# Optimization experiments

Hardware: AMD Instinct MI355X
Metric: run time of the kernel (lower is better)

## Reference

```python
import jax, jax.numpy as jnp
import numpy as np

T, B, I, H = 2048, 64, 256, 256

def setup_inputs() -> dict:
    key = jax.random.key(0)
    k_x, k_wih, k_whh = jax.random.split(key, 3)
    x = jax.random.normal(k_x, (T, B, I), dtype=jnp.float32)
    h0 = jnp.zeros((1, B, H), dtype=jnp.float32)
    # nn.RNN weight_ih_l0 init: U(-1/sqrt(H), 1/sqrt(H)); shape [H, I]
    bound = 1.0 / np.sqrt(H)
    W_ih = jax.random.uniform(k_wih, (H, I), minval=-bound, maxval=bound, dtype=jnp.float32)
    # IndRNN recurrent weight: diagonal vector, U(-1, 1); biases are zeroed.
    w_hh = jax.random.uniform(k_whh, (H,), minval=-1.0, maxval=1.0, dtype=jnp.float32)
    return {"x": x, "h0": h0, "W_ih": W_ih, "w_hh": w_hh}

def reference(x, h0, W_ih, w_hh):
    # Precompute the input projection for all timesteps (the only GEMM):
    # [T, B, H] = x @ W_ih^T  (biases are zero)
    xW = jnp.einsum('tbi,hi->tbh', x, W_ih)

    def step(h, xw_t):
        # IndRNN: diagonal recurrence -> elementwise multiply instead of matmul
        h_new = jax.nn.relu(xw_t + h * w_hh)
        return h_new, h_new

    h_last, outputs = jax.lax.scan(step, h0[0], xW)
    return outputs, h_last[None]  # ([T,B,H], [1,B,H]) matching nn.RNN
```

## Files before the change

### kernel.cpp

```cpp
#include <hip/hip_runtime.h>

typedef short v8s __attribute__((ext_vector_type(8)));
typedef float v4f __attribute__((ext_vector_type(4)));

#define BATCH 16
#define NBATCH 128
#define BH 16384
#define TBH 33554432

__device__ __forceinline__ ushort f2bf(float f) {
  uint u = __float_as_uint(f);
  u += 0x7FFF + ((u >> 16) & 1);
  return (ushort)(u >> 16);
}

__global__ __launch_bounds__(512) void indrnn_gemm(
    const float* __restrict__ A,
    const float* __restrict__ W,
    ushort* __restrict__ C)
{
  __shared__ ushort As[128 * 72];
  __shared__ ushort Bs[256 * 72];

  const int tid  = threadIdx.x;
  const int lane = tid & 63;
  const int wid  = tid >> 6;
  const int wm   = wid >> 2;
  const int wn   = wid & 3;
  const int m0   = blockIdx.x * 128;

  const int l15 = lane & 15;
  const int lhi = lane >> 4;

  v4f acc[4][4] = {};

  for (int kc = 0; kc < 4; ++kc) {
    #pragma unroll
    for (int j = 0; j < 4; ++j) {
      int f    = j * 512 + tid;
      int row  = f >> 4;
      int colf = f & 15;
      const float4 a4 = *(const float4*)(A + ((size_t)(m0 + row) << 8) + kc * 64 + colf * 4);
      ushort4 b4 = make_ushort4(f2bf(a4.x), f2bf(a4.y), f2bf(a4.z), f2bf(a4.w));
      *(ushort4*)(As + row * 72 + colf * 4) = b4;
    }
    #pragma unroll
    for (int j = 0; j < 8; ++j) {
      int f    = j * 512 + tid;
      int row  = f >> 4;
      int colf = f & 15;
      const float4 a4 = *(const float4*)(W + ((size_t)row << 8) + kc * 64 + colf * 4);
      ushort4 b4 = make_ushort4(f2bf(a4.x), f2bf(a4.y), f2bf(a4.z), f2bf(a4.w));
      *(ushort4*)(Bs + row * 72 + colf * 4) = b4;
    }
    __syncthreads();

    #pragma unroll
    for (int kk = 0; kk < 2; ++kk) {
      const int koff = kk * 32 + lhi * 8;
      v8s af[4], bf[4];
      #pragma unroll
      for (int mt = 0; mt < 4; ++mt)
        af[mt] = *(const v8s*)(As + (wm * 64 + mt * 16 + l15) * 72 + koff);
      #pragma unroll
      for (int nt = 0; nt < 4; ++nt)
        bf[nt] = *(const v8s*)(Bs + (wn * 64 + nt * 16 + l15) * 72 + koff);
      #pragma unroll
      for (int mt = 0; mt < 4; ++mt)
        #pragma unroll
        for (int nt = 0; nt < 4; ++nt)
          acc[mt][nt] = __builtin_amdgcn_mfma_f32_16x16x32_bf16(af[mt], bf[nt], acc[mt][nt], 0, 0, 0);
    }
    __syncthreads();
  }

  #pragma unroll
  for (int mt = 0; mt < 4; ++mt) {
    #pragma unroll
    for (int nt = 0; nt < 4; ++nt) {
      #pragma unroll
      for (int r = 0; r < 4; ++r) {
        int row = m0 + wm * 64 + mt * 16 + lhi * 4 + r;
        int col = wn * 64 + nt * 16 + l15;
        C[((size_t)row << 8) + col] = f2bf(acc[mt][nt][r]);
      }
    }
  }
}

__global__ __launch_bounds__(64) void indrnn_scan(
    const ushort* __restrict__ xw,
    const float* __restrict__ h0,
    const float* __restrict__ w_hh,
    float* __restrict__ out)
{
  const int ch = blockIdx.x * 64 + threadIdx.x;
  const float w = w_hh[ch & 255];
  float h = h0[ch];
  const ushort* px = xw + ch;
  float* po = out + ch;

  uint b0[BATCH], b1[BATCH], b2[BATCH], b3[BATCH];

  auto ld = [&](uint (&buf)[BATCH], int kb) {
    const ushort* p = px + (size_t)kb * BATCH * BH;
    #pragma unroll
    for (int j = 0; j < BATCH; ++j) buf[j] = p[(size_t)j * BH];
  };
  auto cp = [&](uint (&buf)[BATCH], int kb) {
    float* o = po + (size_t)kb * BATCH * BH;
    #pragma unroll
    for (int j = 0; j < BATCH; ++j) {
      float xv = __uint_as_float(buf[j] << 16);
      h = fmaxf(fmaf(h, w, xv), 0.0f);
      o[(size_t)j * BH] = h;
    }
  };

  ld(b0, 0); ld(b1, 1); ld(b2, 2); ld(b3, 3);
  for (int kb = 0; kb < NBATCH; kb += 4) {
    cp(b0, kb);     if (kb + 4 < NBATCH) ld(b0, kb + 4);
    cp(b1, kb + 1); if (kb + 5 < NBATCH) ld(b1, kb + 5);
    cp(b2, kb + 2); if (kb + 6 < NBATCH) ld(b2, kb + 6);
    cp(b3, kb + 3); if (kb + 7 < NBATCH) ld(b3, kb + 7);
  }
  out[(size_t)TBH + ch] = h;
}

extern "C" void kernel_launch(void* const* d_in, const int* in_sizes, int n_in,
                              void* d_out, int out_size, void* d_ws, size_t ws_size,
                              hipStream_t stream) {
  const float* x    = (const float*)d_in[0];
  const float* h0   = (const float*)d_in[1];
  const float* W_ih = (const float*)d_in[2];
  const float* w_hh = (const float*)d_in[3];
  float* out = (float*)d_out;
  ushort* xw = (ushort*)d_ws;

  indrnn_gemm<<<dim3(1024), dim3(512), 0, stream>>>(x, W_ih, xw);
  indrnn_scan<<<dim3(256), dim3(64), 0, stream>>>(xw, h0, w_hh, out);
}
```

Measured before the change: 298.9 us.

## Split IndRNN scan into chained time segments and retile GEMM to 128x128

The scan is split into 8 time segments of 256 steps, giving 2048 blocks instead of 256. Each block preloads its whole segment of bf16 projections into registers, then waits for the previous segment's final hidden state. That state is handed over through the output buffer as h+1, which is safe because ReLU keeps h non-negative; the receiver spins with agent-scope atomics until the value is at least 1, then writes back the true value. The GEMM moves to 128x128 tiles with 256 threads and twice as many blocks, to raise occupancy. The goal is to hide the memory latency of the serial scan across many more waves, at the cost of a spin-wait chain whose forward progress depends on blocks being dispatched in order.

Result: slower. 512.9 us (+71.6%).

```diff
diff --git a/kernel.cpp b/kernel.cpp
--- a/kernel.cpp
+++ b/kernel.cpp
@@ -3,10 +3,10 @@
 typedef short v8s __attribute__((ext_vector_type(8)));
 typedef float v4f __attribute__((ext_vector_type(4)));
 
-#define BATCH 16
-#define NBATCH 128
 #define BH 16384
 #define TBH 33554432
+#define TSEG 256
+#define NSEG 8
 
 __device__ __forceinline__ ushort f2bf(float f) {
   uint u = __float_as_uint(f);
@@ -14,20 +14,23 @@
   return (ushort)(u >> 16);
 }
 
-__global__ __launch_bounds__(512) void indrnn_gemm(
+__global__ __launch_bounds__(256, 3) void indrnn_gemm(
     const float* __restrict__ A,
     const float* __restrict__ W,
     ushort* __restrict__ C)
 {
   __shared__ ushort As[128 * 72];
-  __shared__ ushort Bs[256 * 72];
+  __shared__ ushort Bs[128 * 72];
 
   const int tid  = threadIdx.x;
   const int lane = tid & 63;
   const int wid  = tid >> 6;
-  const int wm   = wid >> 2;
-  const int wn   = wid & 3;
-  const int m0   = blockIdx.x * 128;
+  const int wm   = wid >> 1;
+  const int wn   = wid & 1;
+  const int mb   = blockIdx.x >> 1;
+  const int nb   = blockIdx.x & 1;
+  const int m0   = mb * 128;
+  const int n0   = nb * 128;
 
   const int l15 = lane & 15;
   const int lhi = lane >> 4;
@@ -36,22 +39,22 @@
 
   for (int kc = 0; kc < 4; ++kc) {
     #pragma unroll
-    for (int j = 0; j < 4; ++j) {
-      int f    = j * 512 + tid;
+    for (int j = 0; j < 8; ++j) {
+      int f    = j * 256 + tid;
       int row  = f >> 4;
       int colf = f & 15;
       const float4 a4 = *(const float4*)(A + ((size_t)(m0 + row) << 8) + kc * 64 + colf * 4);
-      ushort4 b4 = make_ushort4(f2bf(a4.x), f2bf(a4.y), f2bf(a4.z), f2bf(a4.w));
-      *(ushort4*)(As + row * 72 + colf * 4) = b4;
+      *(ushort4*)(As + row * 72 + colf * 4) =
+          make_ushort4(f2bf(a4.x), f2bf(a4.y), f2bf(a4.z), f2bf(a4.w));
     }
     #pragma unroll
     for (int j = 0; j < 8; ++j) {
-      int f    = j * 512 + tid;
+      int f    = j * 256 + tid;
       int row  = f >> 4;
       int colf = f & 15;
-      const float4 a4 = *(const float4*)(W + ((size_t)row << 8) + kc * 64 + colf * 4);
-      ushort4 b4 = make_ushort4(f2bf(a4.x), f2bf(a4.y), f2bf(a4.z), f2bf(a4.w));
-      *(ushort4*)(Bs + row * 72 + colf * 4) = b4;
+      const float4 a4 = *(const float4*)(W + ((size_t)(n0 + row) << 8) + kc * 64 + colf * 4);
+      *(ushort4*)(Bs + row * 72 + colf * 4) =
+          make_ushort4(f2bf(a4.x), f2bf(a4.y), f2bf(a4.z), f2bf(a4.w));
     }
     __syncthreads();
 
@@ -81,50 +84,68 @@
       #pragma unroll
       for (int r = 0; r < 4; ++r) {
         int row = m0 + wm * 64 + mt * 16 + lhi * 4 + r;
-        int col = wn * 64 + nt * 16 + l15;
+        int col = n0 + wn * 64 + nt * 16 + l15;
         C[((size_t)row << 8) + col] = f2bf(acc[mt][nt][r]);
       }
     }
   }
 }
 
-__global__ __launch_bounds__(64) void indrnn_scan(
+__global__ __launch_bounds__(64, 2) void indrnn_scan(
     const ushort* __restrict__ xw,
     const float* __restrict__ h0,
     const float* __restrict__ w_hh,
     float* __restrict__ out)
 {
-  const int ch = blockIdx.x * 64 + threadIdx.x;
+  const int s  = blockIdx.x >> 8;
+  const int g  = blockIdx.x & 255;
+  const int ch = g * 64 + threadIdx.x;
   const float w = w_hh[ch & 255];
-  float h = h0[ch];
-  const ushort* px = xw + ch;
-  float* po = out + ch;
+  const int t0 = s * TSEG;
+  const ushort* px = xw + (size_t)t0 * BH + ch;
+  float* po = out + (size_t)t0 * BH + ch;
 
-  uint b0[BATCH], b1[BATCH], b2[BATCH], b3[BATCH];
+  uint pk[TSEG / 2];
+  #pragma unroll
+  for (int j = 0; j < TSEG / 2; ++j) {
+    uint lo = px[(size_t)(2 * j) * BH];
+    uint hi = px[(size_t)(2 * j + 1) * BH];
+    pk[j] = lo | (hi << 16);
+  }
 
-  auto ld = [&](uint (&buf)[BATCH], int kb) {
-    const ushort* p = px + (size_t)kb * BATCH * BH;
-    #pragma unroll
-    for (int j = 0; j < BATCH; ++j) buf[j] = p[(size_t)j * BH];
-  };
-  auto cp = [&](uint (&buf)[BATCH], int kb) {
-    float* o = po + (size_t)kb * BATCH * BH;
-    #pragma unroll
-    for (int j = 0; j < BATCH; ++j) {
-      float xv = __uint_as_float(buf[j] << 16);
-      h = fmaxf(fmaf(h, w, xv), 0.0f);
-      o[(size_t)j * BH] = h;
+  float h;
+  if (s == 0) {
+    h = h0[ch];
+  } else {
+    float* sig = out + ((size_t)t0 - 1) * (size_t)BH + ch;
+    float v;
+    do {
+      v = __hip_atomic_load(sig, __ATOMIC_RELAXED, __HIP_MEMORY_SCOPE_AGENT);
+    } while (!(v >= 1.0f));
+    h = v - 1.0f;
+    __hip_atomic_store(sig, h, __ATOMIC_RELAXED, __HIP_MEMORY_SCOPE_AGENT);
+  }
+
+  #pragma unroll
+  for (int j = 0; j < TSEG / 2; ++j) {
+    float x0 = __uint_as_float(pk[j] << 16);
+    h = fmaxf(fmaf(h, w, x0), 0.0f);
+    po[(size_t)(2 * j) * BH] = h;
+
+    float x1 = __uint_as_float(pk[j] & 0xFFFF0000u);
+    h = fmaxf(fmaf(h, w, x1), 0.0f);
+    if (j == TSEG / 2 - 1) {
+      if (s == NSEG - 1) {
+        po[(size_t)(2 * j + 1) * BH] = h;
+        out[(size_t)TBH + ch] = h;
+      } else {
+        __hip_atomic_store(&po[(size_t)(2 * j + 1) * BH], h + 1.0f,
+                           __ATOMIC_RELAXED, __HIP_MEMORY_SCOPE_AGENT);
+      }
+    } else {
+      po[(size_t)(2 * j + 1) * BH] = h;
     }
-  };
-
-  ld(b0, 0); ld(b1, 1); ld(b2, 2); ld(b3, 3);
-  for (int kb = 0; kb < NBATCH; kb += 4) {
-    cp(b0, kb);     if (kb + 4 < NBATCH) ld(b0, kb + 4);
-    cp(b1, kb + 1); if (kb + 5 < NBATCH) ld(b1, kb + 5);
-    cp(b2, kb + 2); if (kb + 6 < NBATCH) ld(b2, kb + 6);
-    cp(b3, kb + 3); if (kb + 7 < NBATCH) ld(b3, kb + 7);
   }
-  out[(size_t)TBH + ch] = h;
 }
 
 extern "C" void kernel_launch(void* const* d_in, const int* in_sizes, int n_in,
@@ -137,6 +158,6 @@
   float* out = (float*)d_out;
   ushort* xw = (ushort*)d_ws;
 
-  indrnn_gemm<<<dim3(1024), dim3(512), 0, stream>>>(x, W_ih, xw);
-  indrnn_scan<<<dim3(256), dim3(64), 0, stream>>>(xw, h0, w_hh, out);
+  indrnn_gemm<<<dim3(2048), dim3(256), 0, stream>>>(x, W_ih, xw);
+  indrnn_scan<<<dim3(2048), dim3(64), 0, stream>>>(xw, h0, w_hh, out);
 }
```

## Warp-specialize scan with LDS double buffering and prefetch GEMM A tiles

Applied to the files above, without the earlier changes.

The scan kernel now uses 256-thread blocks: one wave runs the serial recurrence from LDS while three producer waves stage the next 128-step chunk of xw into LDS and write the previous chunk's outputs to global memory as vectorized float4 stores. This targets the latency-bound serial loop and the per-step strided scalar global loads and stores. The GEMM also prefetches the next K-chunk of A into registers during the MFMA phase. The cost is 48KB of LDS per block and a block-wide barrier per chunk, and the recurrence still runs on only one wave per block.

After: 301.7 us. Within noise of the previous version (+1.0%).

```diff
diff --git a/kernel.cpp b/kernel.cpp
--- a/kernel.cpp
+++ b/kernel.cpp
@@ -3,10 +3,10 @@
 typedef short v8s __attribute__((ext_vector_type(8)));
 typedef float v4f __attribute__((ext_vector_type(4)));
 
-#define BATCH 16
-#define NBATCH 128
 #define BH 16384
 #define TBH 33554432
+#define CT 128
+#define NC 16
 
 __device__ __forceinline__ ushort f2bf(float f) {
   uint u = __float_as_uint(f);
@@ -32,28 +32,42 @@
   const int l15 = lane & 15;
   const int lhi = lane >> 4;
 
+  int arow[4], acolf[4];
+  #pragma unroll
+  for (int j = 0; j < 4; ++j) {
+    int f = j * 512 + tid;
+    arow[j]  = f >> 4;
+    acolf[j] = f & 15;
+  }
+
+  float4 pa[4];
+  #pragma unroll
+  for (int j = 0; j < 4; ++j)
+    pa[j] = *(const float4*)(A + ((size_t)(m0 + arow[j]) << 8) + acolf[j] * 4);
+
   v4f acc[4][4] = {};
 
   for (int kc = 0; kc < 4; ++kc) {
     #pragma unroll
-    for (int j = 0; j < 4; ++j) {
-      int f    = j * 512 + tid;
-      int row  = f >> 4;
-      int colf = f & 15;
-      const float4 a4 = *(const float4*)(A + ((size_t)(m0 + row) << 8) + kc * 64 + colf * 4);
-      ushort4 b4 = make_ushort4(f2bf(a4.x), f2bf(a4.y), f2bf(a4.z), f2bf(a4.w));
-      *(ushort4*)(As + row * 72 + colf * 4) = b4;
-    }
+    for (int j = 0; j < 4; ++j)
+      *(ushort4*)(As + arow[j] * 72 + acolf[j] * 4) =
+          make_ushort4(f2bf(pa[j].x), f2bf(pa[j].y), f2bf(pa[j].z), f2bf(pa[j].w));
     #pragma unroll
     for (int j = 0; j < 8; ++j) {
       int f    = j * 512 + tid;
       int row  = f >> 4;
       int colf = f & 15;
       const float4 a4 = *(const float4*)(W + ((size_t)row << 8) + kc * 64 + colf * 4);
-      ushort4 b4 = make_ushort4(f2bf(a4.x), f2bf(a4.y), f2bf(a4.z), f2bf(a4.w));
-      *(ushort4*)(Bs + row * 72 + colf * 4) = b4;
+      *(ushort4*)(Bs + row * 72 + colf * 4) =
+          make_ushort4(f2bf(a4.x), f2bf(a4.y), f2bf(a4.z), f2bf(a4.w));
     }
     __syncthreads();
+
+    if (kc < 3) {
+      #pragma unroll
+      for (int j = 0; j < 4; ++j)
+        pa[j] = *(const float4*)(A + ((size_t)(m0 + arow[j]) << 8) + (kc + 1) * 64 + acolf[j] * 4);
+    }
 
     #pragma unroll
     for (int kk = 0; kk < 2; ++kk) {
@@ -88,43 +102,79 @@
   }
 }
 
-__global__ __launch_bounds__(64) void indrnn_scan(
+__global__ __launch_bounds__(256) void indrnn_scan(
     const ushort* __restrict__ xw,
     const float* __restrict__ h0,
     const float* __restrict__ w_hh,
     float* __restrict__ out)
 {
-  const int ch = blockIdx.x * 64 + threadIdx.x;
-  const float w = w_hh[ch & 255];
-  float h = h0[ch];
-  const ushort* px = xw + ch;
-  float* po = out + ch;
+  __shared__ alignas(16) ushort xin[2][CT * 64];
+  __shared__ alignas(16) float  xout[2][CT * 64];
 
-  uint b0[BATCH], b1[BATCH], b2[BATCH], b3[BATCH];
+  const int tid  = threadIdx.x;
+  const int wave = tid >> 6;
+  const int lane = tid & 63;
+  const int ch0  = blockIdx.x * 64;
 
-  auto ld = [&](uint (&buf)[BATCH], int kb) {
-    const ushort* p = px + (size_t)kb * BATCH * BH;
-    #pragma unroll
-    for (int j = 0; j < BATCH; ++j) buf[j] = p[(size_t)j * BH];
-  };
-  auto cp = [&](uint (&buf)[BATCH], int kb) {
-    float* o = po + (size_t)kb * BATCH * BH;
-    #pragma unroll
-    for (int j = 0; j < BATCH; ++j) {
-      float xv = __uint_as_float(buf[j] << 16);
-      h = fmaxf(fmaf(h, w, xv), 0.0f);
-      o[(size_t)j * BH] = h;
+  if (wave == 0) {
+    const int ch = ch0 + lane;
+    const float w = w_hh[ch & 255];
+    float h = h0[ch];
+    __syncthreads();
+    for (int c = 0; c < NC; ++c) {
+      const ushort* xi = xin[c & 1];
+      float*        xo = xout[c & 1];
+      #pragma unroll
+      for (int t = 0; t < CT; ++t) {
+        float xv = __uint_as_float(((uint)xi[t * 64 + lane]) << 16);
+        h = fmaxf(fmaf(h, w, xv), 0.0f);
+        xo[t * 64 + lane] = h;
+      }
+      __syncthreads();
     }
-  };
+    out[(size_t)TBH + ch] = h;
+  } else {
+    const int cl = tid - 64;
 
-  ld(b0, 0); ld(b1, 1); ld(b2, 2); ld(b3, 3);
-  for (int kb = 0; kb < NBATCH; kb += 4) {
-    cp(b0, kb);     if (kb + 4 < NBATCH) ld(b0, kb + 4);
-    cp(b1, kb + 1); if (kb + 5 < NBATCH) ld(b1, kb + 5);
-    cp(b2, kb + 2); if (kb + 6 < NBATCH) ld(b2, kb + 6);
-    cp(b3, kb + 3); if (kb + 7 < NBATCH) ld(b3, kb + 7);
+    for (int i = cl; i < CT * 16; i += 192) {
+      int t  = i >> 4;
+      int c4 = (i & 15) * 4;
+      *(ushort4*)(&xin[0][t * 64 + c4]) =
+          *(const ushort4*)(xw + (size_t)t * BH + ch0 + c4);
+    }
+    __syncthreads();
+
+    for (int c = 0; c < NC; ++c) {
+      if (c + 1 < NC) {
+        const ushort* src = xw + (size_t)(c + 1) * CT * BH + ch0;
+        ushort* dst = xin[(c + 1) & 1];
+        for (int i = cl; i < CT * 16; i += 192) {
+          int t  = i >> 4;
+          int c4 = (i & 15) * 4;
+          *(ushort4*)(dst + t * 64 + c4) = *(const ushort4*)(src + (size_t)t * BH + c4);
+        }
+      }
+      if (c > 0) {
+        const float* src = xout[(c - 1) & 1];
+        float* dst = out + (size_t)(c - 1) * CT * BH + ch0;
+        for (int i = cl; i < CT * 16; i += 192) {
+          int t  = i >> 4;
+          int c4 = (i & 15) * 4;
+          *(float4*)(dst + (size_t)t * BH + c4) = *(const float4*)(src + t * 64 + c4);
+        }
+      }
+      __syncthreads();
+    }
+    {
+      const float* src = xout[(NC - 1) & 1];
+      float* dst = out + (size_t)(NC - 1) * CT * BH + ch0;
+      for (int i = cl; i < CT * 16; i += 192) {
+        int t  = i >> 4;
+        int c4 = (i & 15) * 4;
+        *(float4*)(dst + (size_t)t * BH + c4) = *(const float4*)(src + t * 64 + c4);
+      }
+    }
   }
-  out[(size_t)TBH + ch] = h;
 }
 
 extern "C" void kernel_launch(void* const* d_in, const int* in_sizes, int n_in,
@@ -138,5 +188,5 @@
   ushort* xw = (ushort*)d_ws;
 
   indrnn_gemm<<<dim3(1024), dim3(512), 0, stream>>>(x, W_ih, xw);
-  indrnn_scan<<<dim3(256), dim3(64), 0, stream>>>(xw, h0, w_hh, out);
+  indrnn_scan<<<dim3(256), dim3(256), 0, stream>>>(xw, h0, w_hh, out);
 }
```

## Fuse input-projection GEMM and IndRNN scan into one pipelined kernel

Applied to the files above, without the earlier changes.

Replaces the separate GEMM and scan kernels with a single kernel. Each block owns one batch row and 64 hidden channels and computes the projection for 64-timestep chunks into LDS with MFMA. Wave 0 runs the recurrence while the other waves prefetch the next x chunk into a double buffer. This removes the bf16 xW round trip through global memory and one launch, but leaves only 256 blocks, each with a single wave on the serial scan, and puts block barriers between chunks.

After: 546.0 us. 82.7% more time.

```diff
diff --git a/kernel.cpp b/kernel.cpp
--- a/kernel.cpp
+++ b/kernel.cpp
@@ -3,10 +3,12 @@
 typedef short v8s __attribute__((ext_vector_type(8)));
 typedef float v4f __attribute__((ext_vector_type(4)));
 
-#define BATCH 16
-#define NBATCH 128
 #define BH 16384
 #define TBH 33554432
+#define CT 64
+#define NC 32
+#define XP 264
+#define WP 72
 
 __device__ __forceinline__ ushort f2bf(float f) {
   uint u = __float_as_uint(f);
@@ -14,117 +16,120 @@
   return (ushort)(u >> 16);
 }
 
-__global__ __launch_bounds__(512) void indrnn_gemm(
-    const float* __restrict__ A,
+__global__ __launch_bounds__(256) void indrnn_fused(
+    const float* __restrict__ x,
+    const float* __restrict__ h0,
     const float* __restrict__ W,
-    ushort* __restrict__ C)
+    const float* __restrict__ w_hh,
+    float* __restrict__ out)
 {
-  __shared__ ushort As[128 * 72];
-  __shared__ ushort Bs[256 * 72];
+  __shared__ ushort Ws[64 * XP];
+  __shared__ ushort Xs[2][CT * XP];
+  __shared__ float  XWs[CT * WP];
 
   const int tid  = threadIdx.x;
+  const int wave = tid >> 6;
   const int lane = tid & 63;
-  const int wid  = tid >> 6;
-  const int wm   = wid >> 2;
-  const int wn   = wid & 3;
-  const int m0   = blockIdx.x * 128;
+
+  const int xcd  = blockIdx.x & 7;
+  const int q    = blockIdx.x >> 3;
+  const int b    = xcd * 8 + (q >> 2);
+  const int hq   = q & 3;
+  const int base = b * 256 + hq * 64;
 
   const int l15 = lane & 15;
   const int lhi = lane >> 4;
 
-  v4f acc[4][4] = {};
+  for (int i = tid; i < 64 * 64; i += 256) {
+    int r  = i >> 6;
+    int c4 = (i & 63) * 4;
+    float4 a4 = *(const float4*)(W + (size_t)(hq * 64 + r) * 256 + c4);
+    *(ushort4*)(Ws + r * XP + c4) =
+        make_ushort4(f2bf(a4.x), f2bf(a4.y), f2bf(a4.z), f2bf(a4.w));
+  }
+  #pragma unroll
+  for (int pc = 0; pc < 2; ++pc) {
+    const float* src = x + (size_t)pc * CT * BH + b * 256;
+    ushort* dst = Xs[pc];
+    for (int i = tid; i < CT * 64; i += 256) {
+      int t  = i >> 6;
+      int c4 = (i & 63) * 4;
+      float4 a4 = *(const float4*)(src + (size_t)t * BH + c4);
+      *(ushort4*)(dst + t * XP + c4) =
+          make_ushort4(f2bf(a4.x), f2bf(a4.y), f2bf(a4.z), f2bf(a4.w));
+    }
+  }
+  __syncthreads();
 
-  for (int kc = 0; kc < 4; ++kc) {
+  const float w = w_hh[hq * 64 + lane];
+  float h = (wave == 0) ? h0[base + lane] : 0.0f;
+
+  {
+    v4f acc[4] = {};
     #pragma unroll
-    for (int j = 0; j < 4; ++j) {
-      int f    = j * 512 + tid;
-      int row  = f >> 4;
-      int colf = f & 15;
-      const float4 a4 = *(const float4*)(A + ((size_t)(m0 + row) << 8) + kc * 64 + colf * 4);
-      ushort4 b4 = make_ushort4(f2bf(a4.x), f2bf(a4.y), f2bf(a4.z), f2bf(a4.w));
-      *(ushort4*)(As + row * 72 + colf * 4) = b4;
+    for (int kk = 0; kk < 8; ++kk) {
+      const int koff = kk * 32 + lhi * 8;
+      v8s af = *(const v8s*)(Xs[0] + (wave * 16 + l15) * XP + koff);
+      #pragma unroll
+      for (int nt = 0; nt < 4; ++nt) {
+        v8s bf = *(const v8s*)(Ws + (nt * 16 + l15) * XP + koff);
+        acc[nt] = __builtin_amdgcn_mfma_f32_16x16x32_bf16(af, bf, acc[nt], 0, 0, 0);
+      }
     }
     #pragma unroll
-    for (int j = 0; j < 8; ++j) {
-      int f    = j * 512 + tid;
-      int row  = f >> 4;
-      int colf = f & 15;
-      const float4 a4 = *(const float4*)(W + ((size_t)row << 8) + kc * 64 + colf * 4);
-      ushort4 b4 = make_ushort4(f2bf(a4.x), f2bf(a4.y), f2bf(a4.z), f2bf(a4.w));
-      *(ushort4*)(Bs + row * 72 + colf * 4) = b4;
+    for (int nt = 0; nt < 4; ++nt)
+      #pragma unroll
+      for (int r = 0; r < 4; ++r)
+        XWs[(wave * 16 + lhi * 4 + r) * WP + nt * 16 + l15] = acc[nt][r];
+  }
+  __syncthreads();
+
+  for (int c = 0; c < NC; ++c) {
+    if (wave == 0) {
+      float* po = out + (size_t)c * CT * BH + base;
+      #pragma unroll 8
+      for (int t = 0; t < CT; ++t) {
+        float xv = XWs[t * WP + lane];
+        h = fmaxf(fmaf(h, w, xv), 0.0f);
+        po[(size_t)t * BH + lane] = h;
+      }
+    } else if (c + 2 < NC) {
+      const float* src = x + (size_t)(c + 2) * CT * BH + b * 256;
+      ushort* dst = Xs[c & 1];
+      for (int i = tid - 64; i < CT * 64; i += 192) {
+        int t  = i >> 6;
+        int c4 = (i & 63) * 4;
+        float4 a4 = *(const float4*)(src + (size_t)t * BH + c4);
+        *(ushort4*)(dst + t * XP + c4) =
+            make_ushort4(f2bf(a4.x), f2bf(a4.y), f2bf(a4.z), f2bf(a4.w));
+      }
     }
     __syncthreads();
 
-    #pragma unroll
-    for (int kk = 0; kk < 2; ++kk) {
-      const int koff = kk * 32 + lhi * 8;
-      v8s af[4], bf[4];
+    if (c + 1 < NC) {
+      const ushort* xb = Xs[(c + 1) & 1];
+      v4f acc[4] = {};
       #pragma unroll
-      for (int mt = 0; mt < 4; ++mt)
-        af[mt] = *(const v8s*)(As + (wm * 64 + mt * 16 + l15) * 72 + koff);
+      for (int kk = 0; kk < 8; ++kk) {
+        const int koff = kk * 32 + lhi * 8;
+        v8s af = *(const v8s*)(xb + (wave * 16 + l15) * XP + koff);
+        #pragma unroll
+        for (int nt = 0; nt < 4; ++nt) {
+          v8s bf = *(const v8s*)(Ws + (nt * 16 + l15) * XP + koff);
+          acc[nt] = __builtin_amdgcn_mfma_f32_16x16x32_bf16(af, bf, acc[nt], 0, 0, 0);
+        }
+      }
       #pragma unroll
       for (int nt = 0; nt < 4; ++nt)
-        bf[nt] = *(const v8s*)(Bs + (wn * 64 + nt * 16 + l15) * 72 + koff);
-      #pragma unroll
-      for (int mt = 0; mt < 4; ++mt)
         #pragma unroll
-        for (int nt = 0; nt < 4; ++nt)
-          acc[mt][nt] = __builtin_amdgcn_mfma_f32_16x16x32_bf16(af[mt], bf[nt], acc[mt][nt], 0, 0, 0);
+        for (int r = 0; r < 4; ++r)
+          XWs[(wave * 16 + lhi * 4 + r) * WP + nt * 16 + l15] = acc[nt][r];
+      __syncthreads();
     }
-    __syncthreads();
   }
 
-  #pragma unroll
-  for (int mt = 0; mt < 4; ++mt) {
-    #pragma unroll
-    for (int nt = 0; nt < 4; ++nt) {
-      #pragma unroll
-      for (int r = 0; r < 4; ++r) {
-        int row = m0 + wm * 64 + mt * 16 + lhi * 4 + r;
-        int col = wn * 64 + nt * 16 + l15;
-        C[((size_t)row << 8) + col] = f2bf(acc[mt][nt][r]);
-      }
-    }
-  }
-}
-
-__global__ __launch_bounds__(64) void indrnn_scan(
-    const ushort* __restrict__ xw,
-    const float* __restrict__ h0,
-    const float* __restrict__ w_hh,
-    float* __restrict__ out)
-{
-  const int ch = blockIdx.x * 64 + threadIdx.x;
-  const float w = w_hh[ch & 255];
-  float h = h0[ch];
-  const ushort* px = xw + ch;
-  float* po = out + ch;
-
-  uint b0[BATCH], b1[BATCH], b2[BATCH], b3[BATCH];
-
-  auto ld = [&](uint (&buf)[BATCH], int kb) {
-    const ushort* p = px + (size_t)kb * BATCH * BH;
-    #pragma unroll
-    for (int j = 0; j < BATCH; ++j) buf[j] = p[(size_t)j * BH];
-  };
-  auto cp = [&](uint (&buf)[BATCH], int kb) {
-    float* o = po + (size_t)kb * BATCH * BH;
-    #pragma unroll
-    for (int j = 0; j < BATCH; ++j) {
-      float xv = __uint_as_float(buf[j] << 16);
-      h = fmaxf(fmaf(h, w, xv), 0.0f);
-      o[(size_t)j * BH] = h;
-    }
-  };
-
-  ld(b0, 0); ld(b1, 1); ld(b2, 2); ld(b3, 3);
-  for (int kb = 0; kb < NBATCH; kb += 4) {
-    cp(b0, kb);     if (kb + 4 < NBATCH) ld(b0, kb + 4);
-    cp(b1, kb + 1); if (kb + 5 < NBATCH) ld(b1, kb + 5);
-    cp(b2, kb + 2); if (kb + 6 < NBATCH) ld(b2, kb + 6);
-    cp(b3, kb + 3); if (kb + 7 < NBATCH) ld(b3, kb + 7);
-  }
-  out[(size_t)TBH + ch] = h;
+  if (wave == 0)
+    out[(size_t)TBH + base + lane] = h;
 }
 
 extern "C" void kernel_launch(void* const* d_in, const int* in_sizes, int n_in,
@@ -135,8 +140,6 @@
   const float* W_ih = (const float*)d_in[2];
   const float* w_hh = (const float*)d_in[3];
   float* out = (float*)d_out;
-  ushort* xw = (ushort*)d_ws;
 
-  indrnn_gemm<<<dim3(1024), dim3(512), 0, stream>>>(x, W_ih, xw);
-  indrnn_scan<<<dim3(256), dim3(64), 0, stream>>>(xw, h0, w_hh, out);
+  indrnn_fused<<<dim3(256), dim3(256), 0, stream>>>(x, h0, W_ih, w_hh, out);
 }
```
